# Optimization experiments

Hardware: AMD Instinct MI355X
Metric: run time of the kernel (lower is better)

## Reference

```python
import jax, jax.numpy as jnp
import numpy as np

N = 100000  # nodes
E = 600000  # edges
D = 128     # input_dim
H = D // 2  # hidden of MLP head
OUT = 10    # output_dim
EPS = 1e-5
NEG_SLOPE = 0.2


def _p(key, shape, scale):
    return jax.random.normal(key, shape, dtype=jnp.float32) * scale


def setup_inputs() -> dict:
    key = jax.random.key(0)
    ks = jax.random.split(key, 16)
    s = 1.0 / np.sqrt(D)
    return {
        "x": jax.random.normal(ks[0], (N, D), dtype=jnp.float32),
        "edge_index": jax.random.randint(ks[1], (2, E), 0, N, dtype=jnp.int64),
        # SAGEConv: lin_l (applied to mean-aggregated neighbors, has bias), lin_r (root)
        "sage_Wl": _p(ks[2], (D, D), s), "sage_Wr": _p(ks[3], (D, D), s),
        "sage_b": jnp.zeros((D,), jnp.float32),
        # GCNConv
        "gcn_W": _p(ks[4], (D, D), s), "gcn_b": jnp.zeros((D,), jnp.float32),
        # GATConv (heads=1)
        "gat_W": _p(ks[5], (D, D), s),
        "gat_att_src": _p(ks[6], (D,), s), "gat_att_dst": _p(ks[7], (D,), s),
        "gat_b": jnp.zeros((D,), jnp.float32),
        # BatchNorms (batch-stat normalization)
        "bn1_g": jnp.ones((D,), jnp.float32), "bn1_b": jnp.zeros((D,), jnp.float32),
        "bn2_g": jnp.ones((D,), jnp.float32), "bn2_b": jnp.zeros((D,), jnp.float32),
        "bn3_g": jnp.ones((D,), jnp.float32), "bn3_b": jnp.zeros((D,), jnp.float32),
        # MLP head
        "lin1_W": _p(ks[8], (D, H), s), "lin1_b": jnp.zeros((H,), jnp.float32),
        "lin2_W": _p(ks[9], (H, OUT), 1.0 / np.sqrt(H)), "lin2_b": jnp.zeros((OUT,), jnp.float32),
    }


def _bn_relu(x, g, b):
    mu = jnp.mean(x, axis=0)
    var = jnp.mean(jnp.square(x - mu), axis=0)
    return jax.nn.relu((x - mu) * jax.lax.rsqrt(var + EPS) * g + b)


def _sage(x, src, dst, Wl, Wr, b):
    agg = jax.ops.segment_sum(x[src], dst, num_segments=N)          # [N, D]
    cnt = jax.ops.segment_sum(jnp.ones((src.shape[0],), x.dtype), dst, num_segments=N)
    mean = agg / jnp.maximum(cnt, 1.0)[:, None]
    return mean @ Wl + x @ Wr + b


def _gcn(x, src, dst, W, b):
    loop = jnp.arange(N, dtype=src.dtype)
    s = jnp.concatenate([src, loop]); d = jnp.concatenate([dst, loop])
    deg = jax.ops.segment_sum(jnp.ones((d.shape[0],), x.dtype), d, num_segments=N)
    dinv = jnp.where(deg > 0, jax.lax.rsqrt(jnp.maximum(deg, 1.0)), 0.0)
    xw = x @ W
    msg = xw[s] * (dinv[s] * dinv[d])[:, None]
    return jax.ops.segment_sum(msg, d, num_segments=N) + b


def _gat(x, src, dst, W, att_s, att_d, b):
    loop = jnp.arange(N, dtype=src.dtype)
    s = jnp.concatenate([src, loop]); d = jnp.concatenate([dst, loop])
    xw = x @ W                                  # [N, D]
    a_s = xw @ att_s                            # [N]
    a_d = xw @ att_d                            # [N]
    e = jax.nn.leaky_relu(a_s[s] + a_d[d], NEG_SLOPE)  # [E+N]
    m = jax.ops.segment_max(e, d, num_segments=N)
    ee = jnp.exp(e - m[d])
    z = jax.ops.segment_sum(ee, d, num_segments=N)
    alpha = ee / z[d]
    return jax.ops.segment_sum(alpha[:, None] * xw[s], d, num_segments=N) + b


def reference(x, edge_index, sage_Wl, sage_Wr, sage_b, gcn_W, gcn_b,
              gat_W, gat_att_src, gat_att_dst, gat_b,
              bn1_g, bn1_b, bn2_g, bn2_b, bn3_g, bn3_b,
              lin1_W, lin1_b, lin2_W, lin2_b):
    src, dst = edge_index[0], edge_index[1]
    h = _bn_relu(_sage(x, src, dst, sage_Wl, sage_Wr, sage_b), bn1_g, bn1_b)
    h = _bn_relu(_gcn(h, src, dst, gcn_W, gcn_b), bn2_g, bn2_b)
    h = _bn_relu(_gat(h, src, dst, gat_W, gat_att_src, gat_att_dst, gat_b), bn3_g, bn3_b)
    # dropout is identity in eval mode
    h = jax.nn.relu(h @ lin1_W + lin1_b) @ lin2_W + lin2_b
    return jax.nn.log_softmax(h, axis=1)
```

## Files before the change

### kernel.cpp

```cpp
#include <hip/hip_runtime.h>

static constexpr int Dd = 128;
static constexpr int Hh = 64;
static constexpr int OC = 10;
#define CDIV(a,b) (((a)+(b)-1)/(b))

typedef __attribute__((ext_vector_type(8))) short short8v;
typedef __attribute__((ext_vector_type(16))) float f32x16;
typedef unsigned short u16;

__device__ __forceinline__ float lrelu(float x){ return x>0.f? x : 0.2f*x; }
__device__ __forceinline__ unsigned f2bf(float f){
  unsigned u = __float_as_uint(f);
  return (u + 0x7FFFu + ((u>>16)&1u)) >> 16;
}
__device__ __forceinline__ float bl(unsigned u){ return __uint_as_float(u<<16); }
__device__ __forceinline__ float bh(unsigned u){ return __uint_as_float(u & 0xFFFF0000u); }

__global__ __launch_bounds__(256) void k_hist(const int* __restrict__ dst, int E,
    int* __restrict__ cnt) {
  int e = blockIdx.x*256 + threadIdx.x;
  if (e < E) atomicAdd(cnt + dst[e], 1);
}

__global__ __launch_bounds__(256) void k_scan_l1(const int* __restrict__ cnt,
    int* __restrict__ rp, int n, int* __restrict__ bsum) {
  __shared__ int sdata[256];
  int t = threadIdx.x;
  int base = blockIdx.x*2048 + t*8;
  int v[8]; int s = 0;
  #pragma unroll
  for (int k = 0; k < 8; k++) { v[k] = (base+k < n) ? cnt[base+k] : 0; s += v[k]; }
  sdata[t] = s; __syncthreads();
  for (int off = 1; off < 256; off <<= 1) {
    int a = sdata[t];
    int b = (t >= off) ? sdata[t-off] : 0;
    __syncthreads();
    sdata[t] = a + b;
    __syncthreads();
  }
  int ex = sdata[t] - s;
  if (t == 255) bsum[blockIdx.x] = sdata[255];
  int run = ex;
  #pragma unroll
  for (int k = 0; k < 8; k++) { if (base+k < n) rp[base+k] = run; run += v[k]; }
}

__global__ void k_scan_l2(int* __restrict__ bsum, int nb) {
  if (threadIdx.x == 0 && blockIdx.x == 0) {
    int run = 0;
    for (int i = 0; i < nb; i++) { int v = bsum[i]; bsum[i] = run; run += v; }
  }
}

__global__ __launch_bounds__(256) void k_scan_l3(int* __restrict__ rp, int n,
    const int* __restrict__ bsum, int E) {
  int off = bsum[blockIdx.x];
  int base = blockIdx.x*2048 + threadIdx.x*8;
  #pragma unroll
  for (int k = 0; k < 8; k++) if (base+k < n) rp[base+k] += off;
  if (blockIdx.x == 0 && threadIdx.x == 0) rp[n] = E;
}

__global__ __launch_bounds__(256) void k_fill(const int* __restrict__ src,
    const int* __restrict__ dst, int E, const int* __restrict__ rp,
    int* __restrict__ cnt, int* __restrict__ col) {
  int e = blockIdx.x*256 + threadIdx.x;
  if (e >= E) return;
  int d = dst[e];
  int pos = rp[d] + atomicSub(cnt + d, 1) - 1;
  col[pos] = src[e];
}

__global__ __launch_bounds__(256) void k_dinv(const int* __restrict__ rp,
    float* __restrict__ dinv, int n) {
  int i = blockIdx.x*256 + threadIdx.x;
  if (i < n) dinv[i] = rsqrtf((float)(rp[i+1] - rp[i]) + 1.0f);
}

__global__ __launch_bounds__(256) void k_wt_all(
    const float* __restrict__ w0, const float* __restrict__ w1,
    const float* __restrict__ w2, const float* __restrict__ w3,
    const float* __restrict__ w4,
    u16* __restrict__ o0, u16* __restrict__ o1, u16* __restrict__ o2,
    u16* __restrict__ o3, u16* __restrict__ o4) {
  int idx = blockIdx.x*256 + threadIdx.x;
  const float* W; u16* O; int base, N;
  if (idx < 65536) {
    int m = idx >> 14;
    W = m==0?w0 : m==1?w1 : m==2?w2 : w3;
    O = m==0?o0 : m==1?o1 : m==2?o2 : o3;
    base = idx & 16383; N = 128;
  } else if (idx < 73728) {
    W = w4; O = o4; base = idx - 65536; N = 64;
  } else return;
  int n = base / 128, k = base % 128;
  int kc = k >> 3, nf = n >> 5, lm = n & 31;
  int fi = (((kc*(N>>5) + nf)*32 + lm) << 3) | (k & 7);
  O[fi] = (u16)f2bf(W[k*N + n]);
}

__global__ __launch_bounds__(256) void k_tobf16(const float* __restrict__ in,
    u16* __restrict__ out, int n8) {
  int idx = blockIdx.x*256 + threadIdx.x;
  if (idx >= n8) return;
  const float4* p = reinterpret_cast<const float4*>(in) + idx*2;
  float4 v0 = p[0], v1 = p[1];
  uint4 w;
  w.x = f2bf(v0.x) | (f2bf(v0.y)<<16);
  w.y = f2bf(v0.z) | (f2bf(v0.w)<<16);
  w.z = f2bf(v1.x) | (f2bf(v1.y)<<16);
  w.w = f2bf(v1.z) | (f2bf(v1.w)<<16);
  reinterpret_cast<uint4*>(out)[idx] = w;
}

__global__ __launch_bounds__(256) void k_sage_gather(const u16* __restrict__ xb,
    const int* __restrict__ rp, const int* __restrict__ col,
    u16* __restrict__ ob, int n) {
  int gid = blockIdx.x*256 + threadIdx.x;
  int i = gid >> 5, l = gid & 31;
  if (i >= n) return;
  int beg = rp[i], end = rp[i+1];
  const u16* xp = xb + l*4;
  float a0=0.f, a1=0.f, a2=0.f, a3=0.f;
  int j = beg;
  for (; j+4 <= end; j += 4) {
    int s0=col[j], s1=col[j+1], s2=col[j+2], s3=col[j+3];
    uint2 v0 = *reinterpret_cast<const uint2*>(xp + (size_t)s0*Dd);
    uint2 v1 = *reinterpret_cast<const uint2*>(xp + (size_t)s1*Dd);
    uint2 v2 = *reinterpret_cast<const uint2*>(xp + (size_t)s2*Dd);
    uint2 v3 = *reinterpret_cast<const uint2*>(xp + (size_t)s3*Dd);
    a0 += (bl(v0.x)+bl(v1.x)) + (bl(v2.x)+bl(v3.x));
    a1 += (bh(v0.x)+bh(v1.x)) + (bh(v2.x)+bh(v3.x));
    a2 += (bl(v0.y)+bl(v1.y)) + (bl(v2.y)+bl(v3.y));
    a3 += (bh(v0.y)+bh(v1.y)) + (bh(v2.y)+bh(v3.y));
  }
  for (; j < end; j++) {
    int s = col[j];
    uint2 v = *reinterpret_cast<const uint2*>(xp + (size_t)s*Dd);
    a0 += bl(v.x); a1 += bh(v.x); a2 += bl(v.y); a3 += bh(v.y);
  }
  float inv = 1.0f / fmaxf((float)(end - beg), 1.0f);
  uint2 o;
  o.x = f2bf(a0*inv) | (f2bf(a1*inv)<<16);
  o.y = f2bf(a2*inv) | (f2bf(a3*inv)<<16);
  *reinterpret_cast<uint2*>(ob + (size_t)i*Dd + l*4) = o;
}

__global__ __launch_bounds__(256) void k_gcn_gather(const u16* __restrict__ xb,
    const int* __restrict__ rp, const int* __restrict__ col,
    const float* __restrict__ dinv, u16* __restrict__ ob, int n) {
  int gid = blockIdx.x*256 + threadIdx.x;
  int i = gid >> 5, l = gid & 31;
  if (i >= n) return;
  int beg = rp[i], end = rp[i+1];
  const u16* xp = xb + l*4;
  float a0=0.f, a1=0.f, a2=0.f, a3=0.f;
  int j = beg;
  for (; j+4 <= end; j += 4) {
    int s0=col[j], s1=col[j+1], s2=col[j+2], s3=col[j+3];
    uint2 v0 = *reinterpret_cast<const uint2*>(xp + (size_t)s0*Dd);
    uint2 v1 = *reinterpret_cast<const uint2*>(xp + (size_t)s1*Dd);
    uint2 v2 = *reinterpret_cast<const uint2*>(xp + (size_t)s2*Dd);
    uint2 v3 = *reinterpret_cast<const uint2*>(xp + (size_t)s3*Dd);
    float w0 = dinv[s0], w1 = dinv[s1], w2 = dinv[s2], w3 = dinv[s3];
    a0 += (w0*bl(v0.x)+w1*bl(v1.x)) + (w2*bl(v2.x)+w3*bl(v3.x));
    a1 += (w0*bh(v0.x)+w1*bh(v1.x)) + (w2*bh(v2.x)+w3*bh(v3.x));
    a2 += (w0*bl(v0.y)+w1*bl(v1.y)) + (w2*bl(v2.y)+w3*bl(v3.y));
    a3 += (w0*bh(v0.y)+w1*bh(v1.y)) + (w2*bh(v2.y)+w3*bh(v3.y));
  }
  for (; j < end; j++) {
    int s = col[j];
    float w = dinv[s];
    uint2 v = *reinterpret_cast<const uint2*>(xp + (size_t)s*Dd);
    a0 += w*bl(v.x); a1 += w*bh(v.x); a2 += w*bl(v.y); a3 += w*bh(v.y);
  }
  float di = dinv[i];
  float ws = di*di;
  uint2 sv = *reinterpret_cast<const uint2*>(xp + (size_t)i*Dd);
  a0 = di*a0 + ws*bl(sv.x); a1 = di*a1 + ws*bh(sv.x);
  a2 = di*a2 + ws*bl(sv.y); a3 = di*a3 + ws*bh(sv.y);
  uint2 o;
  o.x = f2bf(a0) | (f2bf(a1)<<16);
  o.y = f2bf(a2) | (f2bf(a3)<<16);
  *reinterpret_cast<uint2*>(ob + (size_t)i*Dd + l*4) = o;
}

__global__ __launch_bounds__(256) void k_gat_gather(const u16* __restrict__ xb,
    const int* __restrict__ rp, const int* __restrict__ col,
    const float* __restrict__ a_s, const float* __restrict__ a_d,
    u16* __restrict__ ob, int n) {
  int gid = blockIdx.x*256 + threadIdx.x;
  int i = gid >> 5, l = gid & 31;
  if (i >= n) return;
  int beg = rp[i], end = rp[i+1];
  const u16* xp = xb + l*4;
  float ad = a_d[i];
  float m = lrelu(a_s[i] + ad);
  float z = 1.0f;
  uint2 sv = *reinterpret_cast<const uint2*>(xp + (size_t)i*Dd);
  float a0 = bl(sv.x), a1 = bh(sv.x), a2 = bl(sv.y), a3 = bh(sv.y);
  int j = beg;
  for (; j+4 <= end; j += 4) {
    int s0=col[j], s1=col[j+1], s2=col[j+2], s3=col[j+3];
    uint2 v0 = *reinterpret_cast<const uint2*>(xp + (size_t)s0*Dd);
    uint2 v1 = *reinterpret_cast<const uint2*>(xp + (size_t)s1*Dd);
    uint2 v2 = *reinterpret_cast<const uint2*>(xp + (size_t)s2*Dd);
    uint2 v3 = *reinterpret_cast<const uint2*>(xp + (size_t)s3*Dd);
    float e0 = lrelu(a_s[s0]+ad), e1 = lrelu(a_s[s1]+ad);
    float e2 = lrelu(a_s[s2]+ad), e3 = lrelu(a_s[s3]+ad);
    float mg = fmaxf(fmaxf(e0,e1), fmaxf(e2,e3));
    if (mg > m) {
      float r = __expf(m - mg);
      z *= r; a0 *= r; a1 *= r; a2 *= r; a3 *= r;
      m = mg;
    }
    float w0 = __expf(e0-m), w1 = __expf(e1-m);
    float w2 = __expf(e2-m), w3 = __expf(e3-m);
    z += (w0+w1) + (w2+w3);
    a0 += (w0*bl(v0.x)+w1*bl(v1.x)) + (w2*bl(v2.x)+w3*bl(v3.x));
    a1 += (w0*bh(v0.x)+w1*bh(v1.x)) + (w2*bh(v2.x)+w3*bh(v3.x));
    a2 += (w0*bl(v0.y)+w1*bl(v1.y)) + (w2*bl(v2.y)+w3*bl(v3.y));
    a3 += (w0*bh(v0.y)+w1*bh(v1.y)) + (w2*bh(v2.y)+w3*bh(v3.y));
  }
  for (; j < end; j++) {
    int s = col[j];
    uint2 v = *reinterpret_cast<const uint2*>(xp + (size_t)s*Dd);
    float e = lrelu(a_s[s]+ad);
    if (e > m) {
      float r = __expf(m - e);
      z *= r; a0 *= r; a1 *= r; a2 *= r; a3 *= r;
      m = e;
    }
    float w = __expf(e-m);
    z += w;
    a0 += w*bl(v.x); a1 += w*bh(v.x); a2 += w*bl(v.y); a3 += w*bh(v.y);
  }
  float inv = 1.0f / z;
  uint2 o;
  o.x = f2bf(a0*inv) | (f2bf(a1*inv)<<16);
  o.y = f2bf(a2*inv) | (f2bf(a3*inv)<<16);
  *reinterpret_cast<uint2*>(ob + (size_t)i*Dd + l*4) = o;
}

__global__ __launch_bounds__(256) void k_bn_stats_bf(const u16* __restrict__ X, int M,
    float* __restrict__ gsum, float* __restrict__ gsq) {
  __shared__ float ss[2][256];
  int t = threadIdx.x;
  int cd = t & 63;
  int rg = t >> 6;
  float s0=0.f, q0=0.f, s1=0.f, q1=0.f;
  const unsigned* Xu = reinterpret_cast<const unsigned*>(X);
  for (int r = blockIdx.x*4 + rg; r < M; r += gridDim.x*4) {
    unsigned v = Xu[(size_t)r*64 + cd];
    float a = bl(v), b = bh(v);
    s0 += a; q0 += a*a; s1 += b; q1 += b*b;
  }
  ss[0][t] = s0; ss[1][t] = q0; __syncthreads();
  float rs0 = 0.f, rq0 = 0.f;
  if (rg == 0) {
    rs0 = ss[0][cd] + ss[0][cd+64] + ss[0][cd+128] + ss[0][cd+192];
    rq0 = ss[1][cd] + ss[1][cd+64] + ss[1][cd+128] + ss[1][cd+192];
  }
  __syncthreads();
  ss[0][t] = s1; ss[1][t] = q1; __syncthreads();
  if (rg == 0) {
    float rs1 = ss[0][cd] + ss[0][cd+64] + ss[0][cd+128] + ss[0][cd+192];
    float rq1 = ss[1][cd] + ss[1][cd+64] + ss[1][cd+128] + ss[1][cd+192];
    atomicAdd(gsum + 2*cd,     rs0); atomicAdd(gsq + 2*cd,     rq0);
    atomicAdd(gsum + 2*cd + 1, rs1); atomicAdd(gsq + 2*cd + 1, rq1);
  }
}

template<int NCOLS, bool DUAL, bool BNA, bool STATS, bool BIASRELU, bool ATT, bool OUTBF, bool HEAD>
__global__ __launch_bounds__(256) void k_mm(
    const u16* __restrict__ A1, const u16* __restrict__ A2,
    const u16* __restrict__ WT1, const u16* __restrict__ WT2,
    const float* __restrict__ bng, const float* __restrict__ bnb,
    const float* __restrict__ bsum_in, const float* __restrict__ bsq_in,
    const float* __restrict__ bias,
    void* __restrict__ Cout, int M,
    float* __restrict__ gsum, float* __restrict__ gsq,
    const float* __restrict__ att_sv, const float* __restrict__ att_dv,
    float* __restrict__ as_out, float* __restrict__ ad_out,
    const float* __restrict__ W2, const float* __restrict__ b2) {
  constexpr int NF = NCOLS/32;
  __shared__ char ldsA[128*272];
  __shared__ char ldsW[NCOLS*256];
  __shared__ float s_scale[128], s_shift[128];
  __shared__ float s_sum[128], s_sq[128];
  __shared__ float w2s[Hh][OC];
  __shared__ float b2s[OC];
  int t = threadIdx.x;
  int wave = t >> 6, l = t & 63;
  int lm = l & 31, h = l >> 5;
  int row0 = blockIdx.x*128;

  if constexpr (BNA) {
    if (t < 128) {
      float mu = bsum_in[t] / (float)M;
      float var = fmaxf(bsq_in[t] / (float)M - mu*mu, 0.f);
      float sc = bng[t] * rsqrtf(var + 1e-5f);
      s_scale[t] = sc;
      s_shift[t] = bnb[t] - mu*sc;
    }
  }
  if constexpr (STATS) {
    if (t < 128) { s_sum[t] = 0.f; s_sq[t] = 0.f; }
  }
  if constexpr (HEAD) {
    for (int i = t; i < Hh*OC; i += 256) w2s[i/OC][i%OC] = W2[i];
    if (t < OC) b2s[t] = b2[t];
  }
  if (BNA || STATS || HEAD) __syncthreads();

  f32x16 acc[NF];
  #pragma unroll
  for (int nf = 0; nf < NF; nf++)
    #pragma unroll
    for (int i = 0; i < 16; i++) acc[nf][i] = 0.f;

  const int nph = DUAL ? 2 : 1;
  for (int ph = 0; ph < nph; ph++) {
    if (ph) __syncthreads();
    const u16* A = (DUAL && ph) ? A2 : A1;
    const u16* WT = (DUAL && ph) ? WT2 : WT1;
    #pragma unroll
    for (int i = 0; i < 8; i++) {
      int c = i*256 + t; int row = c >> 4; int k0 = (c & 15) << 3;
      uint4 w = {0,0,0,0};
      if (row0 + row < M)
        w = *reinterpret_cast<const uint4*>(A + (size_t)(row0+row)*128 + k0);
      if constexpr (BNA) {
        float4 sc0 = *reinterpret_cast<const float4*>(&s_scale[k0]);
        float4 sc1 = *reinterpret_cast<const float4*>(&s_scale[k0+4]);
        float4 sh0 = *reinterpret_cast<const float4*>(&s_shift[k0]);
        float4 sh1 = *reinterpret_cast<const float4*>(&s_shift[k0+4]);
        float e0 = fmaxf(bl(w.x)*sc0.x+sh0.x, 0.f), e1 = fmaxf(bh(w.x)*sc0.y+sh0.y, 0.f);
        float e2 = fmaxf(bl(w.y)*sc0.z+sh0.z, 0.f), e3 = fmaxf(bh(w.y)*sc0.w+sh0.w, 0.f);
        float e4 = fmaxf(bl(w.z)*sc1.x+sh1.x, 0.f), e5 = fmaxf(bh(w.z)*sc1.y+sh1.y, 0.f);
        float e6 = fmaxf(bl(w.w)*sc1.z+sh1.z, 0.f), e7 = fmaxf(bh(w.w)*sc1.w+sh1.w, 0.f);
        w.x = f2bf(e0) | (f2bf(e1)<<16);
        w.y = f2bf(e2) | (f2bf(e3)<<16);
        w.z = f2bf(e4) | (f2bf(e5)<<16);
        w.w = f2bf(e6) | (f2bf(e7)<<16);
      }
      *reinterpret_cast<uint4*>(ldsA + row*272 + k0*2) = w;
    }
    #pragma unroll
    for (int i = 0; i < NCOLS/16; i++) {
      int c = i*256 + t;
      reinterpret_cast<uint4*>(ldsW)[c] = reinterpret_cast<const uint4*>(WT)[c];
    }
    __syncthreads();
    #pragma unroll
    for (int ks = 0; ks < 8; ks++) {
      int kc = ks*2 + h;
      int arow = wave*32 + lm;
      short8v af = *reinterpret_cast<short8v*>(ldsA + arow*272 + kc*16);
      #pragma unroll
      for (int nf = 0; nf < NF; nf++) {
        short8v bf = *reinterpret_cast<short8v*>(ldsW + ((kc*NF + nf)*32 + lm)*16);
        acc[nf] = __builtin_amdgcn_mfma_f32_32x32x16_bf16(af, bf, acc[nf], 0, 0, 0);
      }
    }
  }
  if constexpr (HEAD) {
    __syncthreads();
    float* mrow = reinterpret_cast<float*>(ldsA);
    #pragma unroll
    for (int nf = 0; nf < NF; nf++) {
      int colg = nf*32 + lm;
      float bv = bias[colg];
      #pragma unroll
      for (int reg = 0; reg < 16; reg++) {
        int row = wave*32 + (reg&3) + 8*(reg>>2) + 4*h;
        mrow[row*65 + colg] = fmaxf(acc[nf][reg] + bv, 0.f);
      }
    }
    __syncthreads();
    if (t < 128) {
      int row = row0 + t;
      if (row < M) {
        float p[OC];
        #pragma unroll
        for (int c = 0; c < OC; c++) p[c] = b2s[c];
        for (int k = 0; k < Hh; k++) {
          float a = mrow[t*65 + k];
          #pragma unroll
          for (int c = 0; c < OC; c++) p[c] += a * w2s[k][c];
        }
        float mx = p[0];
        #pragma unroll
        for (int c = 1; c < OC; c++) mx = fmaxf(mx, p[c]);
        float s = 0.f;
        #pragma unroll
        for (int c = 0; c < OC; c++) s += __expf(p[c] - mx);
        float lse = mx + __logf(s);
        #pragma unroll
        for (int c = 0; c < OC; c++)
          ((float*)Cout)[(size_t)row*OC + c] = p[c] - lse;
      }
    }
    return;
  }
  #pragma unroll
  for (int nf = 0; nf < NF; nf++) {
    int colg = nf*32 + lm;
    float bv = 0.f;
    if constexpr (BIASRELU) bv = bias[colg];
    float ps = 0.f, pq = 0.f;
    #pragma unroll
    for (int reg = 0; reg < 16; reg++) {
      int row = row0 + wave*32 + (reg&3) + 8*(reg>>2) + 4*h;
      float v = acc[nf][reg];
      if constexpr (BIASRELU) v = fmaxf(v + bv, 0.f);
      if (row < M) {
        if constexpr (OUTBF)
          ((u16*)Cout)[(size_t)row*NCOLS + colg] = (u16)f2bf(v);
        else
          ((float*)Cout)[(size_t)row*NCOLS + colg] = v;
      }
      ps += v; pq += v*v;
    }
    if constexpr (STATS) {
      atomicAdd(&s_sum[colg], ps);
      atomicAdd(&s_sq[colg], pq);
    }
  }
  if constexpr (ATT) {
    float as_c[NF], ad_c[NF];
    #pragma unroll
    for (int nf = 0; nf < NF; nf++) { as_c[nf] = att_sv[nf*32+lm]; ad_c[nf] = att_dv[nf*32+lm]; }
    #pragma unroll
    for (int reg = 0; reg < 16; reg++) {
      float ps = 0.f, pd = 0.f;
      #pragma unroll
      for (int nf = 0; nf < NF; nf++) { float v = acc[nf][reg]; ps += v*as_c[nf]; pd += v*ad_c[nf]; }
      #pragma unroll
      for (int mm = 1; mm < 32; mm <<= 1) { ps += __shfl_xor(ps, mm); pd += __shfl_xor(pd, mm); }
      int row = row0 + wave*32 + (reg&3) + 8*(reg>>2) + 4*h;
      if (lm == 0 && row < M) { as_out[row] = ps; ad_out[row] = pd; }
    }
  }
  if constexpr (STATS) {
    __syncthreads();
    if (t < 128) { atomicAdd(gsum + t, s_sum[t]); atomicAdd(gsq + t, s_sq[t]); }
  }
}

extern "C" void kernel_launch(void* const* d_in, const int* in_sizes, int n_in,
                              void* d_out, int out_size, void* d_ws, size_t ws_size,
                              hipStream_t stream) {
  const float* x       = (const float*)d_in[0];
  const int*   ei      = (const int*)d_in[1];
  const float* sage_Wl = (const float*)d_in[2];
  const float* sage_Wr = (const float*)d_in[3];
  const float* gcn_W   = (const float*)d_in[5];
  const float* gat_W   = (const float*)d_in[7];
  const float* att_s   = (const float*)d_in[8];
  const float* att_d   = (const float*)d_in[9];
  const float* bn1_g = (const float*)d_in[11], *bn1_b = (const float*)d_in[12];
  const float* bn2_g = (const float*)d_in[13], *bn2_b = (const float*)d_in[14];
  const float* bn3_g = (const float*)d_in[15], *bn3_b = (const float*)d_in[16];
  const float* lin1_W = (const float*)d_in[17], *lin1_b = (const float*)d_in[18];
  const float* lin2_W = (const float*)d_in[19], *lin2_b = (const float*)d_in[20];

  const int Nn = in_sizes[0] / Dd;
  const int Ee = in_sizes[1] / 2;
  const int* srcv = ei;
  const int* dstv = ei + Ee;

  u16* b0 = (u16*)d_ws;
  u16* b1 = b0 + (size_t)Nn*Dd;
  u16* b2 = b1 + (size_t)Nn*Dd;
  float* dinv  = (float*)(b2 + (size_t)Nn*Dd);
  float* a_s   = dinv + Nn;
  float* a_d   = a_s + Nn;
  float* bs    = a_d + Nn;
  float* bs1_sum = bs,        *bs1_sq = bs + 128;
  float* bs2_sum = bs + 256,  *bs2_sq = bs + 384;
  float* bs3_sum = bs + 512,  *bs3_sq = bs + 640;
  int* rp    = (int*)(bs + 768);
  int* cnt_i = rp + (Nn + 1);
  int* bsum  = cnt_i + Nn;
  int* col   = bsum + 64;
  u16* wt_sWl = (u16*)(col + Ee);
  u16* wt_sWr = wt_sWl + 128*128;
  u16* wt_gcn = wt_sWr + 128*128;
  u16* wt_gat = wt_gcn + 128*128;
  u16* wt_l1  = wt_gat + 128*128;

  const dim3 B(256);
  const dim3 Gn(CDIV(Nn, 256));
  const dim3 Gn32(CDIV(Nn*32, 256));
  const dim3 Ge(CDIV(Ee, 256));
  const dim3 Gmm(CDIV(Nn, 128));
  const dim3 Gstat(512);
  const int nscan = CDIV(Nn, 2048);

  hipMemsetAsync(cnt_i, 0, (size_t)Nn*sizeof(int), stream);
  hipMemsetAsync(bs, 0, 768*sizeof(float), stream);

  k_hist<<<Ge, B, 0, stream>>>(dstv, Ee, cnt_i);
  k_scan_l1<<<dim3(nscan), B, 0, stream>>>(cnt_i, rp, Nn, bsum);
  k_scan_l2<<<dim3(1), dim3(64), 0, stream>>>(bsum, nscan);
  k_scan_l3<<<dim3(nscan), B, 0, stream>>>(rp, Nn, bsum, Ee);
  k_fill<<<Ge, B, 0, stream>>>(srcv, dstv, Ee, rp, cnt_i, col);
  k_dinv<<<Gn, B, 0, stream>>>(rp, dinv, Nn);
  k_wt_all<<<dim3(288), B, 0, stream>>>(sage_Wl, sage_Wr, gcn_W, gat_W, lin1_W,
                                        wt_sWl, wt_sWr, wt_gcn, wt_gat, wt_l1);
  k_tobf16<<<dim3(CDIV(Nn*Dd/8, 256)), B, 0, stream>>>(x, b0, Nn*Dd/8);

  k_sage_gather<<<Gn32, B, 0, stream>>>(b0, rp, col, b1, Nn);
  k_mm<128, true, false, true, false, false, true, false><<<Gmm, B, 0, stream>>>(
      b1, b0, wt_sWl, wt_sWr, nullptr, nullptr, nullptr, nullptr, nullptr,
      b2, Nn, bs1_sum, bs1_sq, nullptr, nullptr, nullptr, nullptr, nullptr, nullptr);

  k_mm<128, false, true, false, false, false, true, false><<<Gmm, B, 0, stream>>>(
      b2, nullptr, wt_gcn, nullptr, bn1_g, bn1_b, bs1_sum, bs1_sq, nullptr,
      b0, Nn, nullptr, nullptr, nullptr, nullptr, nullptr, nullptr, nullptr, nullptr);
  k_gcn_gather<<<Gn32, B, 0, stream>>>(b0, rp, col, dinv, b1, Nn);
  k_bn_stats_bf<<<Gstat, B, 0, stream>>>(b1, Nn, bs2_sum, bs2_sq);

  k_mm<128, false, true, false, false, true, true, false><<<Gmm, B, 0, stream>>>(
      b1, nullptr, wt_gat, nullptr, bn2_g, bn2_b, bs2_sum, bs2_sq, nullptr,
      b2, Nn, nullptr, nullptr, att_s, att_d, a_s, a_d, nullptr, nullptr);
  k_gat_gather<<<Gn32, B, 0, stream>>>(b2, rp, col, a_s, a_d, b0, Nn);
  k_bn_stats_bf<<<Gstat, B, 0, stream>>>(b0, Nn, bs3_sum, bs3_sq);

  k_mm<64, false, true, false, true, false, false, true><<<Gmm, B, 0, stream>>>(
      b0, nullptr, wt_l1, nullptr, bn3_g, bn3_b, bs3_sum, bs3_sq, lin1_b,
      (float*)d_out, Nn, nullptr, nullptr, nullptr, nullptr, nullptr, nullptr,
      lin2_W, lin2_b);
}
```

Before: 381.9 us.

## Halve k_mm row tile to 64 and split waves 2x2 over rows and columns

The fused matmul kernel now processes 64 rows per block instead of 128. The four waves are arranged as 2 row halves by 2 column halves, so each wave holds half as many MFMA accumulators. LDS is cut by shrinking the A tile and merging the auxiliary arrays into one buffer. The HEAD path now reads W2 and b2 straight from global memory, and attention logits are combined across column-half waves with LDS atomics. This doubles the grid size and lowers register and LDS pressure, aiming for better occupancy and load balance across CUs. The cost is loading the weight tile twice as often per row and adding extra syncs.

Result: slower. 394.5 us (+3.3%).

```diff
diff --git a/kernel.cpp b/kernel.cpp
--- a/kernel.cpp
+++ b/kernel.cpp
@@ -284,39 +284,34 @@
     const float* __restrict__ att_sv, const float* __restrict__ att_dv,
     float* __restrict__ as_out, float* __restrict__ ad_out,
     const float* __restrict__ W2, const float* __restrict__ b2) {
-  constexpr int NF = NCOLS/32;
-  __shared__ char ldsA[128*272];
+  constexpr int NF  = NCOLS/32;
+  constexpr int NFW = NF/2;
+  __shared__ char ldsA[64*272];
   __shared__ char ldsW[NCOLS*256];
-  __shared__ float s_scale[128], s_shift[128];
-  __shared__ float s_sum[128], s_sq[128];
-  __shared__ float w2s[Hh][OC];
-  __shared__ float b2s[OC];
+  __shared__ float s_aux[256];
   int t = threadIdx.x;
   int wave = t >> 6, l = t & 63;
   int lm = l & 31, h = l >> 5;
-  int row0 = blockIdx.x*128;
+  int rhalf = wave & 1, chalf = wave >> 1;
+  int row0 = blockIdx.x*64;
 
   if constexpr (BNA) {
     if (t < 128) {
       float mu = bsum_in[t] / (float)M;
       float var = fmaxf(bsq_in[t] / (float)M - mu*mu, 0.f);
       float sc = bng[t] * rsqrtf(var + 1e-5f);
-      s_scale[t] = sc;
-      s_shift[t] = bnb[t] - mu*sc;
+      s_aux[t] = sc;
+      s_aux[128 + t] = bnb[t] - mu*sc;
     }
   }
   if constexpr (STATS) {
-    if (t < 128) { s_sum[t] = 0.f; s_sq[t] = 0.f; }
-  }
-  if constexpr (HEAD) {
-    for (int i = t; i < Hh*OC; i += 256) w2s[i/OC][i%OC] = W2[i];
-    if (t < OC) b2s[t] = b2[t];
-  }
-  if (BNA || STATS || HEAD) __syncthreads();
-
-  f32x16 acc[NF];
+    s_aux[t] = 0.f;
+  }
+  if (BNA || STATS) __syncthreads();
+
+  f32x16 acc[NFW];
   #pragma unroll
-  for (int nf = 0; nf < NF; nf++)
+  for (int nf = 0; nf < NFW; nf++)
     #pragma unroll
     for (int i = 0; i < 16; i++) acc[nf][i] = 0.f;
 
@@ -326,16 +321,16 @@
     const u16* A = (DUAL && ph) ? A2 : A1;
     const u16* WT = (DUAL && ph) ? WT2 : WT1;
     #pragma unroll
-    for (int i = 0; i < 8; i++) {
+    for (int i = 0; i < 4; i++) {
       int c = i*256 + t; int row = c >> 4; int k0 = (c & 15) << 3;
       uint4 w = {0,0,0,0};
       if (row0 + row < M)
         w = *reinterpret_cast<const uint4*>(A + (size_t)(row0+row)*128 + k0);
       if constexpr (BNA) {
-        float4 sc0 = *reinterpret_cast<const float4*>(&s_scale[k0]);
-        float4 sc1 = *reinterpret_cast<const float4*>(&s_scale[k0+4]);
-        float4 sh0 = *reinterpret_cast<const float4*>(&s_shift[k0]);
-        float4 sh1 = *reinterpret_cast<const float4*>(&s_shift[k0+4]);
+        float4 sc0 = *reinterpret_cast<const float4*>(&s_aux[k0]);
+        float4 sc1 = *reinterpret_cast<const float4*>(&s_aux[k0+4]);
+        float4 sh0 = *reinterpret_cast<const float4*>(&s_aux[128+k0]);
+        float4 sh1 = *reinterpret_cast<const float4*>(&s_aux[128+k0+4]);
         float e0 = fmaxf(bl(w.x)*sc0.x+sh0.x, 0.f), e1 = fmaxf(bh(w.x)*sc0.y+sh0.y, 0.f);
         float e2 = fmaxf(bl(w.y)*sc0.z+sh0.z, 0.f), e3 = fmaxf(bh(w.y)*sc0.w+sh0.w, 0.f);
         float e4 = fmaxf(bl(w.z)*sc1.x+sh1.x, 0.f), e5 = fmaxf(bh(w.z)*sc1.y+sh1.y, 0.f);
@@ -356,39 +351,39 @@
     #pragma unroll
     for (int ks = 0; ks < 8; ks++) {
       int kc = ks*2 + h;
-      int arow = wave*32 + lm;
+      int arow = rhalf*32 + lm;
       short8v af = *reinterpret_cast<short8v*>(ldsA + arow*272 + kc*16);
       #pragma unroll
-      for (int nf = 0; nf < NF; nf++) {
+      for (int nfw = 0; nfw < NFW; nfw++) {
+        int nf = chalf*NFW + nfw;
         short8v bf = *reinterpret_cast<short8v*>(ldsW + ((kc*NF + nf)*32 + lm)*16);
-        acc[nf] = __builtin_amdgcn_mfma_f32_32x32x16_bf16(af, bf, acc[nf], 0, 0, 0);
+        acc[nfw] = __builtin_amdgcn_mfma_f32_32x32x16_bf16(af, bf, acc[nfw], 0, 0, 0);
       }
     }
   }
   if constexpr (HEAD) {
     __syncthreads();
     float* mrow = reinterpret_cast<float*>(ldsA);
-    #pragma unroll
-    for (int nf = 0; nf < NF; nf++) {
-      int colg = nf*32 + lm;
+    {
+      int colg = chalf*32 + lm;
       float bv = bias[colg];
       #pragma unroll
       for (int reg = 0; reg < 16; reg++) {
-        int row = wave*32 + (reg&3) + 8*(reg>>2) + 4*h;
-        mrow[row*65 + colg] = fmaxf(acc[nf][reg] + bv, 0.f);
+        int rowl = rhalf*32 + (reg&3) + 8*(reg>>2) + 4*h;
+        mrow[rowl*65 + colg] = fmaxf(acc[0][reg] + bv, 0.f);
       }
     }
     __syncthreads();
-    if (t < 128) {
+    if (t < 64) {
       int row = row0 + t;
       if (row < M) {
         float p[OC];
         #pragma unroll
-        for (int c = 0; c < OC; c++) p[c] = b2s[c];
+        for (int c = 0; c < OC; c++) p[c] = b2[c];
         for (int k = 0; k < Hh; k++) {
           float a = mrow[t*65 + k];
           #pragma unroll
-          for (int c = 0; c < OC; c++) p[c] += a * w2s[k][c];
+          for (int c = 0; c < OC; c++) p[c] += a * W2[k*OC + c];
         }
         float mx = p[0];
         #pragma unroll
@@ -405,15 +400,15 @@
     return;
   }
   #pragma unroll
-  for (int nf = 0; nf < NF; nf++) {
-    int colg = nf*32 + lm;
+  for (int nfw = 0; nfw < NFW; nfw++) {
+    int colg = (chalf*NFW + nfw)*32 + lm;
     float bv = 0.f;
     if constexpr (BIASRELU) bv = bias[colg];
     float ps = 0.f, pq = 0.f;
     #pragma unroll
     for (int reg = 0; reg < 16; reg++) {
-      int row = row0 + wave*32 + (reg&3) + 8*(reg>>2) + 4*h;
-      float v = acc[nf][reg];
+      int row = row0 + rhalf*32 + (reg&3) + 8*(reg>>2) + 4*h;
+      float v = acc[nfw][reg];
       if constexpr (BIASRELU) v = fmaxf(v + bv, 0.f);
       if (row < M) {
         if constexpr (OUTBF)
@@ -424,28 +419,41 @@
       ps += v; pq += v*v;
     }
     if constexpr (STATS) {
-      atomicAdd(&s_sum[colg], ps);
-      atomicAdd(&s_sq[colg], pq);
+      atomicAdd(&s_aux[colg], ps);
+      atomicAdd(&s_aux[128 + colg], pq);
     }
   }
   if constexpr (ATT) {
-    float as_c[NF], ad_c[NF];
-    #pragma unroll
-    for (int nf = 0; nf < NF; nf++) { as_c[nf] = att_sv[nf*32+lm]; ad_c[nf] = att_dv[nf*32+lm]; }
+    __syncthreads();
+    if (t < 128) s_aux[t] = 0.f;
+    __syncthreads();
+    float as_c[NFW], ad_c[NFW];
+    #pragma unroll
+    for (int nfw = 0; nfw < NFW; nfw++) {
+      int colg = (chalf*NFW + nfw)*32 + lm;
+      as_c[nfw] = att_sv[colg]; ad_c[nfw] = att_dv[colg];
+    }
     #pragma unroll
     for (int reg = 0; reg < 16; reg++) {
       float ps = 0.f, pd = 0.f;
       #pragma unroll
-      for (int nf = 0; nf < NF; nf++) { float v = acc[nf][reg]; ps += v*as_c[nf]; pd += v*ad_c[nf]; }
+      for (int nfw = 0; nfw < NFW; nfw++) {
+        float v = acc[nfw][reg]; ps += v*as_c[nfw]; pd += v*ad_c[nfw];
+      }
       #pragma unroll
       for (int mm = 1; mm < 32; mm <<= 1) { ps += __shfl_xor(ps, mm); pd += __shfl_xor(pd, mm); }
-      int row = row0 + wave*32 + (reg&3) + 8*(reg>>2) + 4*h;
-      if (lm == 0 && row < M) { as_out[row] = ps; ad_out[row] = pd; }
+      int rowl = rhalf*32 + (reg&3) + 8*(reg>>2) + 4*h;
+      if (lm == 0) { atomicAdd(&s_aux[rowl], ps); atomicAdd(&s_aux[64 + rowl], pd); }
+    }
+    __syncthreads();
+    if (t < 64 && row0 + t < M) {
+      as_out[row0 + t] = s_aux[t];
+      ad_out[row0 + t] = s_aux[64 + t];
     }
   }
   if constexpr (STATS) {
     __syncthreads();
-    if (t < 128) { atomicAdd(gsum + t, s_sum[t]); atomicAdd(gsq + t, s_sq[t]); }
+    if (t < 128) { atomicAdd(gsum + t, s_aux[t]); atomicAdd(gsq + t, s_aux[128 + t]); }
   }
 }
 
@@ -495,7 +503,7 @@
   const dim3 Gn(CDIV(Nn, 256));
   const dim3 Gn32(CDIV(Nn*32, 256));
   const dim3 Ge(CDIV(Ee, 256));
-  const dim3 Gmm(CDIV(Nn, 128));
+  const dim3 Gmm(CDIV(Nn, 64));
   const dim3 Gstat(512);
   const int nscan = CDIV(Nn, 2048);
 
```
